# Performance work log

Hardware: AMD Instinct MI355X
Metric: run time of the kernel (lower is better)

Reference implementation:

```python
import jax, jax.numpy as jnp
import numpy as np

S, B, D, H = 256, 32, 512, 512

def setup_inputs() -> dict:
    key = jax.random.key(0)
    ks = jax.random.split(key, 14)
    return {
        "x": jax.random.normal(ks[0], (S, B, D), jnp.float32),
        "hidden_prev": jax.random.normal(ks[1], (1, B, H), jnp.float32) * 0.1,
        "Z_state": jax.random.normal(ks[2], (1, B, H, D), jnp.float32) * 0.01,
        "F_state": jax.random.normal(ks[3], (1, B, H, D), jnp.float32) * 0.01,
        "wz_state": jax.random.normal(ks[4], (1, B, H), jnp.float32) * 0.01,
        "wf_state": jax.random.normal(ks[5], (1, B, H), jnp.float32) * 0.01,
        "bz_state": jax.random.normal(ks[6], (1, B, H), jnp.float32) * 0.01,
        "bf_state": jax.random.normal(ks[7], (1, B, H), jnp.float32) * 0.01,
        "wm_z": jax.random.normal(ks[8], (H, D), jnp.float32) * 0.1,
        "wm_f": jax.random.normal(ks[9], (H, D), jnp.float32) * 0.1,
        "wv_z": jax.random.normal(ks[10], (1, H), jnp.float32) * 0.1,
        "wv_f": jax.random.normal(ks[11], (1, H), jnp.float32) * 0.1,
        "bias_z": jax.random.normal(ks[12], (1, H), jnp.float32) * 0.1,
        "bias_f": jax.random.normal(ks[13], (1, H), jnp.float32) * 0.1,
    }

def reference(x, hidden_prev, Z_state, F_state, wz_state, wf_state, bz_state, bf_state,
              wm_z, wm_f, wv_z, wv_f, bias_z, bias_f):
    # Input projections for both gates, done once: [S,B,H]
    pre_z = jnp.einsum('sbd,hd->sbh', x, wm_z)
    pre_f = jnp.einsum('sbd,hd->sbh', x, wm_f)

    def step(carry, inp):
        cell, Z, Fm, wz, wf, bz, bf = carry
        x_t, pz, pf = inp  # [B,D], [B,H], [B,H]
        z = jnp.tanh(pz + wv_z * cell + bias_z)          # [B,H]
        f = jax.nn.sigmoid(pf + wv_f * cell + bias_f)    # [B,H]
        zf = (1.0 - f) * (1.0 - z * z)
        fz = (cell - z) * (1.0 - f) * f
        common = f + zf * wv_z + fz * wv_f
        # RTRL sensitivity updates (outer products over [B,H,D])
        Zn = common[..., None] * Z + zf[..., None] * x_t[:, None, :]
        Fn = common[..., None] * Fm + fz[..., None] * x_t[:, None, :]
        wzn = cell * zf + common * wz
        wfn = cell * fz + common * wf
        bzn = zf + common * bz
        bfn = fz + common * bf
        new_cell = cell * f + (1.0 - f) * z
        return (new_cell, Zn, Fn, wzn, wfn, bzn, bfn), new_cell

    carry0 = (hidden_prev[0], Z_state[0], F_state[0],
              wz_state[0], wf_state[0], bz_state[0], bf_state[0])
    carry, cells = jax.lax.scan(step, carry0, (x, pre_z, pre_f))
    new_cell, Zn, Fn, wzn, wfn, bzn, bfn = carry
    return (cells, new_cell[None], Zn[None], Fn[None],
            wzn[None], wfn[None], bzn[None], bfn[None])
```

## Files before the change

### kernel.cpp

```cpp
#include <hip/hip_runtime.h>
#include <hip/hip_bf16.h>
#include <math.h>

namespace {

typedef short short8 __attribute__((ext_vector_type(8)));
typedef float floatx4 __attribute__((ext_vector_type(4)));
typedef unsigned int uint32;
typedef unsigned short u16;
typedef unsigned long long u64;

constexpr int S = 256, B = 32, D = 512, H = 512;
constexpr int BH = B * H;
constexpr int M1 = S * B;
constexpr int SBH = S * BH;

__device__ __forceinline__ int swz(int row, int col8) {
  return row * 64 + (col8 ^ ((row & 7) << 3));
}

__device__ __forceinline__ uint32 pkbf(float lo, float hi) {
  __hip_bfloat162 h = __float22bfloat162_rn(make_float2(lo, hi));
  uint32 r;
  __builtin_memcpy(&r, &h, 4);
  return r;
}

__device__ __forceinline__ float fast_sigmoid(float x) {
  float e = __expf(-x);
  return __builtin_amdgcn_rcpf(1.0f + e);
}
__device__ __forceinline__ float fast_tanh(float x) {
  float e = __expf(-2.0f * x);
  return fmaf(2.0f, __builtin_amdgcn_rcpf(1.0f + e), -1.0f);
}

__global__ __launch_bounds__(256) void proj_gemm(
    const float* __restrict__ x, const float* __restrict__ wmz,
    const float* __restrict__ wmf, float2* __restrict__ pzf) {
  __shared__ u16 As[128 * 64];
  __shared__ u16 Bzs[64 * 64];
  __shared__ u16 Bfs[64 * 64];
  const int tid = threadIdx.x;
  const int m0 = blockIdx.x * 128;
  const int n0 = blockIdx.y * 64;
  const int w = tid >> 6, l = tid & 63;
  const int lr = l & 15, lg = l >> 4;
  floatx4 accz[2][4], accf[2][4];
#pragma unroll
  for (int m = 0; m < 2; ++m)
#pragma unroll
    for (int n = 0; n < 4; ++n) {
      accz[m][n] = 0;
      accf[m][n] = 0;
    }
  const int sr = tid >> 3;
  const int sc = (tid & 7) * 8;
  for (int k0 = 0; k0 < D; k0 += 64) {
    __syncthreads();
#pragma unroll
    for (int p = 0; p < 4; ++p) {
      const int r = sr + 32 * p;
      const float* xp = &x[(size_t)(m0 + r) * D + k0 + sc];
      float4 a = *(const float4*)xp;
      float4 b = *(const float4*)(xp + 4);
      uint4 o;
      o.x = pkbf(a.x, a.y);
      o.y = pkbf(a.z, a.w);
      o.z = pkbf(b.x, b.y);
      o.w = pkbf(b.z, b.w);
      *(uint4*)&As[swz(r, sc)] = o;
    }
#pragma unroll
    for (int p = 0; p < 2; ++p) {
      const int r = sr + 32 * p;
      const float* zp = &wmz[(size_t)(n0 + r) * D + k0 + sc];
      float4 a = *(const float4*)zp;
      float4 b = *(const float4*)(zp + 4);
      uint4 o;
      o.x = pkbf(a.x, a.y);
      o.y = pkbf(a.z, a.w);
      o.z = pkbf(b.x, b.y);
      o.w = pkbf(b.z, b.w);
      *(uint4*)&Bzs[swz(r, sc)] = o;
      const float* fp = &wmf[(size_t)(n0 + r) * D + k0 + sc];
      float4 c = *(const float4*)fp;
      float4 d = *(const float4*)(fp + 4);
      uint4 q;
      q.x = pkbf(c.x, c.y);
      q.y = pkbf(c.z, c.w);
      q.z = pkbf(d.x, d.y);
      q.w = pkbf(d.z, d.w);
      *(uint4*)&Bfs[swz(r, sc)] = q;
    }
    __syncthreads();
    __builtin_amdgcn_s_setprio(1);
#pragma unroll
    for (int kk = 0; kk < 2; ++kk) {
      const int kb = kk * 32 + lg * 8;
      short8 a0 = *(const short8*)&As[swz(32 * w + lr, kb)];
      short8 a1 = *(const short8*)&As[swz(32 * w + 16 + lr, kb)];
#pragma unroll
      for (int n = 0; n < 4; ++n) {
        short8 bz = *(const short8*)&Bzs[swz(16 * n + lr, kb)];
        short8 bf = *(const short8*)&Bfs[swz(16 * n + lr, kb)];
        accz[0][n] = __builtin_amdgcn_mfma_f32_16x16x32_bf16(a0, bz, accz[0][n], 0, 0, 0);
        accz[1][n] = __builtin_amdgcn_mfma_f32_16x16x32_bf16(a1, bz, accz[1][n], 0, 0, 0);
        accf[0][n] = __builtin_amdgcn_mfma_f32_16x16x32_bf16(a0, bf, accf[0][n], 0, 0, 0);
        accf[1][n] = __builtin_amdgcn_mfma_f32_16x16x32_bf16(a1, bf, accf[1][n], 0, 0, 0);
      }
    }
    __builtin_amdgcn_s_setprio(0);
  }
#pragma unroll
  for (int m = 0; m < 2; ++m)
#pragma unroll
    for (int n = 0; n < 4; ++n)
#pragma unroll
      for (int j = 0; j < 4; ++j) {
        int row = m0 + 32 * w + 16 * m + lg * 4 + j;
        int col = n0 + 16 * n + lr;
        pzf[(size_t)row * H + col] = make_float2(accz[m][n][j], accf[m][n][j]);
      }
}

#define STEP_BODY(J)                                                       \
    const float z = fast_tanh(fmaf(wvz, cell, pzv));                       \
    const float f = fast_sigmoid(fmaf(wvf, cell, pfv));                    \
    const float zf = (1.0f - f) * (1.0f - z * z);                          \
    const float fz = (cell - z) * (1.0f - f) * f;                          \
    const float common = f + zf * wvz + fz * wvf;                          \
    wz = fmaf(common, wz, cell * zf);                                      \
    wf = fmaf(common, wf, cell * fz);                                      \
    bz = fmaf(common, bz, zf);                                             \
    bf = fmaf(common, bf, fz);                                             \
    cell = fmaf(f, cell - z, z);                                           \
    const size_t ti = (size_t)(t0 + (J)) * BH;                             \
    __builtin_nontemporal_store(cell, cp + ti);                            \
    pz[ti] = make_float2(__uint_as_float(pkbf(zf, fz)), common);

#define STEP_L(J, Q)                                                       \
  {                                                                        \
    const float pzv = Q.x + bsz, pfv = Q.y + bsf;                          \
    Q = pz[(size_t)(t0 + 16 + (J)) * BH];                                  \
    STEP_BODY(J)                                                           \
  }

#define STEP_N(J, Q)                                                       \
  {                                                                        \
    const float pzv = Q.x + bsz, pfv = Q.y + bsf;                          \
    STEP_BODY(J)                                                           \
  }

__global__ __launch_bounds__(64, 1) void scan_fwd(
    const float* __restrict__ hidden_prev, const float* __restrict__ wz0,
    const float* __restrict__ wf0, const float* __restrict__ bz0,
    const float* __restrict__ bf0, const float* __restrict__ wvz_,
    const float* __restrict__ wvf_, const float* __restrict__ bsz_,
    const float* __restrict__ bsf_, float2* pzf_,
    float* __restrict__ out_cells, float* __restrict__ out_newcell,
    float* __restrict__ out_wzn, float* __restrict__ out_wfn,
    float* __restrict__ out_bzn, float* __restrict__ out_bfn) {
  const int bh = blockIdx.x * 64 + threadIdx.x;
  const int h = bh & (H - 1);
  float cell = hidden_prev[bh];
  float wz = wz0[bh], wf = wf0[bh], bz = bz0[bh], bf = bf0[bh];
  const float wvz = wvz_[h], wvf = wvf_[h], bsz = bsz_[h], bsf = bsf_[h];
  float2* pz = pzf_ + bh;
  float* cp = out_cells + bh;

  float2 q0 = pz[(size_t)0 * BH], q1 = pz[(size_t)1 * BH];
  float2 q2 = pz[(size_t)2 * BH], q3 = pz[(size_t)3 * BH];
  float2 q4 = pz[(size_t)4 * BH], q5 = pz[(size_t)5 * BH];
  float2 q6 = pz[(size_t)6 * BH], q7 = pz[(size_t)7 * BH];
  float2 q8 = pz[(size_t)8 * BH], q9 = pz[(size_t)9 * BH];
  float2 q10 = pz[(size_t)10 * BH], q11 = pz[(size_t)11 * BH];
  float2 q12 = pz[(size_t)12 * BH], q13 = pz[(size_t)13 * BH];
  float2 q14 = pz[(size_t)14 * BH], q15 = pz[(size_t)15 * BH];

  for (int t0 = 0; t0 < S - 16; t0 += 16) {
    STEP_L(0, q0)  STEP_L(1, q1)  STEP_L(2, q2)  STEP_L(3, q3)
    STEP_L(4, q4)  STEP_L(5, q5)  STEP_L(6, q6)  STEP_L(7, q7)
    STEP_L(8, q8)  STEP_L(9, q9)  STEP_L(10, q10) STEP_L(11, q11)
    STEP_L(12, q12) STEP_L(13, q13) STEP_L(14, q14) STEP_L(15, q15)
  }
  {
    const int t0 = S - 16;
    STEP_N(0, q0)  STEP_N(1, q1)  STEP_N(2, q2)  STEP_N(3, q3)
    STEP_N(4, q4)  STEP_N(5, q5)  STEP_N(6, q6)  STEP_N(7, q7)
    STEP_N(8, q8)  STEP_N(9, q9)  STEP_N(10, q10) STEP_N(11, q11)
    STEP_N(12, q12) STEP_N(13, q13) STEP_N(14, q14) STEP_N(15, q15)
  }
  out_newcell[bh] = cell;
  out_wzn[bh] = wz;
  out_wfn[bh] = wf;
  out_bzn[bh] = bz;
  out_bfn[bh] = bf;
}

__global__ __launch_bounds__(1024) void suffix_kernel(
    const float2* __restrict__ pzfc, const float* __restrict__ x,
    u16* __restrict__ XT, u16* __restrict__ AzT, u16* __restrict__ AfT,
    float* __restrict__ P0_out) {
  __shared__ union {
    struct {
      float prods[16][65];
      uint32 tl[S * 65];
    } s;
    float xp[4][64][65];
  } u;
  const int tid = threadIdx.x;
  const int bh_l = tid & 63;
  const int c = tid >> 6;

  {
    const int team = tid >> 8;
    const int tt = tid & 255;
    const int tile = blockIdx.x * 4 + team;
    const int b = tile >> 5;
    const int rem = tile & 31;
    const int d0 = (rem >> 2) * 64;
    const int s0 = (rem & 3) * 64;
    const int r = tt >> 4;
    const int c4 = (tt & 15) * 4;
#pragma unroll
    for (int p = 0; p < 4; ++p) {
      const int rr = r + p * 16;
      float4 v = *(const float4*)&x[(size_t)(s0 + rr) * (B * D) +
                                    (size_t)b * D + d0 + c4];
      u.xp[team][c4 + 0][rr] = v.x;
      u.xp[team][c4 + 1][rr] = v.y;
      u.xp[team][c4 + 2][rr] = v.z;
      u.xp[team][c4 + 3][rr] = v.w;
    }
    __syncthreads();
#pragma unroll
    for (int p = 0; p < 4; ++p) {
      const int dr = r + p * 16;
      u64 o = (u64)pkbf(u.xp[team][dr][c4 + 0], u.xp[team][dr][c4 + 1]) |
              ((u64)pkbf(u.xp[team][dr][c4 + 2], u.xp[team][dr][c4 + 3]) << 32);
      *(u64*)&XT[((size_t)b * D + d0 + dr) * S + s0 + c4] = o;
    }
  }
  __syncthreads();

  const int bh = blockIdx.x * 64 + bh_l;
  const float2* p = pzfc + bh;
  float2 v[16];
#pragma unroll
  for (int i = 0; i < 16; ++i) v[i] = p[(size_t)(c * 16 + i) * BH];
  float L = 1.0f;
#pragma unroll
  for (int i = 0; i < 16; ++i) L *= v[i].y;
  u.s.prods[c][bh_l] = L;
  __syncthreads();
  float run = 1.0f;
#pragma unroll
  for (int cc = 1; cc < 16; ++cc)
    if (cc > c) run *= u.s.prods[cc][bh_l];
#pragma unroll
  for (int i = 15; i >= 0; --i) {
    const int t = c * 16 + i;
    const uint32 w32 = __float_as_uint(v[i].x);
    const float zf = __uint_as_float((w32 & 0xffffu) << 16);
    const float fz = __uint_as_float(w32 & 0xffff0000u);
    u.s.tl[t * 65 + bh_l] = pkbf(zf * run, fz * run);
    run *= v[i].y;
  }
  if (c == 0) P0_out[bh] = run;
  __syncthreads();

  const size_t base = (size_t)blockIdx.x * 64 * S;
  const int rot = (bh_l >> 3) & 3;
#pragma unroll
  for (int it = 0; it < 4; ++it) {
    const int qi = it * 1024 + tid;
    const int r = qi >> 6;
    const int qt = (qi & 63) * 4;
    uint32 a[4];
#pragma unroll
    for (int m = 0; m < 4; ++m) {
      const int k = (m + rot) & 3;
      a[k] = u.s.tl[(qt + k) * 65 + r];
    }
    u64 lo = (u64)(a[0] & 0xffffu) | ((u64)(a[1] & 0xffffu) << 16) |
             ((u64)(a[2] & 0xffffu) << 32) | ((u64)(a[3] & 0xffffu) << 48);
    u64 hi = (u64)(a[0] >> 16) | ((u64)(a[1] >> 16) << 16) |
             ((u64)(a[2] >> 16) << 32) | ((u64)(a[3] >> 16) << 48);
    *(u64*)&AzT[base + (size_t)r * S + qt] = lo;
    *(u64*)&AfT[base + (size_t)r * S + qt] = hi;
  }
}

__global__ __launch_bounds__(256, 3) void out_gemm(
    const u16* __restrict__ AzT, const u16* __restrict__ AfT,
    const u16* __restrict__ XT, const float* __restrict__ P0,
    const float* __restrict__ Z0, const float* __restrict__ F0,
    float* __restrict__ Zn, float* __restrict__ Fn) {
  __shared__ u16 smem[(128 + 64) * 64];
  const int tid = threadIdx.x;
  const int fid = blockIdx.x;
  const int L = (fid & 7) * 256 + (fid >> 3);
  const int d0 = (L & 7) * 64;
  const int h0 = ((L >> 3) & 3) * 128;
  const int bz = L >> 5;
  const int b = bz >> 1;
  const u16* A = ((bz & 1) ? AfT : AzT) + (size_t)b * H * S;
  const float* C0 = (bz & 1) ? F0 : Z0;
  float* Cn = (bz & 1) ? Fn : Zn;
  const u16* Xb = XT + (size_t)b * D * S;
  const int w = tid >> 6, l = tid & 63;
  const int lr = l & 15, lg = l >> 4;
  floatx4 acc[2][4];
#pragma unroll
  for (int m = 0; m < 2; ++m)
#pragma unroll
    for (int n = 0; n < 4; ++n) acc[m][n] = 0;
  const int sr = tid >> 3;
  const int sc = (tid & 7) * 8;

  short8 rA[4], rX[2];

#define OG_LOAD(T0)                                                        \
  {                                                                        \
    _Pragma("unroll") for (int p = 0; p < 4; ++p) {                        \
      const int r = sr + 32 * p;                                           \
      rA[p] = *(const short8*)&A[(size_t)(h0 + r) * S + (T0) + sc];        \
    }                                                                      \
    _Pragma("unroll") for (int p = 0; p < 2; ++p) {                        \
      const int r = sr + 32 * p;                                           \
      rX[p] = *(const short8*)&Xb[(size_t)(d0 + r) * S + (T0) + sc];       \
    }                                                                      \
  }

#define OG_WRITE()                                                         \
  {                                                                        \
    u16* As_ = smem;                                                       \
    u16* Xs_ = smem + 128 * 64;                                            \
    _Pragma("unroll") for (int p = 0; p < 4; ++p) {                        \
      const int r = sr + 32 * p;                                           \
      *(short8*)&As_[swz(r, sc)] = rA[p];                                  \
    }                                                                      \
    _Pragma("unroll") for (int p = 0; p < 2; ++p) {                        \
      const int r = sr + 32 * p;                                           \
      *(short8*)&Xs_[swz(r, sc)] = rX[p];                                  \
    }                                                                      \
  }

#define OG_COMPUTE()                                                       \
  {                                                                        \
    const u16* As_ = smem;                                                 \
    const u16* Xs_ = smem + 128 * 64;                                      \
    __builtin_amdgcn_s_setprio(1);                                         \
    _Pragma("unroll") for (int kk = 0; kk < 2; ++kk) {                     \
      const int kb = kk * 32 + lg * 8;                                     \
      short8 a0 = *(const short8*)&As_[swz(32 * w + lr, kb)];              \
      short8 a1 = *(const short8*)&As_[swz(32 * w + 16 + lr, kb)];         \
      _Pragma("unroll") for (int n = 0; n < 4; ++n) {                      \
        short8 xf = *(const short8*)&Xs_[swz(16 * n + lr, kb)];            \
        acc[0][n] = __builtin_amdgcn_mfma_f32_16x16x32_bf16(a0, xf, acc[0][n], 0, 0, 0); \
        acc[1][n] = __builtin_amdgcn_mfma_f32_16x16x32_bf16(a1, xf, acc[1][n], 0, 0, 0); \
      }                                                                    \
    }                                                                      \
    __builtin_amdgcn_s_setprio(0);                                         \
  }

  OG_LOAD(0)
  OG_WRITE()
  __syncthreads();
  OG_LOAD(64)
  OG_COMPUTE()
  __syncthreads();
  OG_WRITE()
  __syncthreads();
  OG_LOAD(128)
  OG_COMPUTE()
  __syncthreads();
  OG_WRITE()
  __syncthreads();
  OG_LOAD(192)
  OG_COMPUTE()
  __syncthreads();
  OG_WRITE()
  __syncthreads();

  floatx4 c0v[8];
  float p0v[8];
#pragma unroll
  for (int half = 0; half < 2; ++half)
#pragma unroll
    for (int i = 0; i < 4; ++i) {
      const int id = i * 256 + tid;
      const int row = half * 64 + (id >> 4);
      const int c4 = (id & 15) * 4;
      const int h = h0 + row;
      p0v[half * 4 + i] = P0[b * H + h];
      c0v[half * 4 + i] = __builtin_nontemporal_load(
          (const floatx4*)&C0[((size_t)b * H + h) * D + d0 + c4]);
    }

  OG_COMPUTE()

  float* eps = (float*)smem;
#pragma unroll
  for (int half = 0; half < 2; ++half) {
    __syncthreads();
    if ((w >> 1) == half) {
      const int lw = w & 1;
#pragma unroll
      for (int m = 0; m < 2; ++m)
#pragma unroll
        for (int n = 0; n < 4; ++n)
#pragma unroll
          for (int j = 0; j < 4; ++j) {
            const int row = 32 * lw + 16 * m + lg * 4 + j;
            eps[row * 68 + 16 * n + lr] = acc[m][n][j];
          }
    }
    __syncthreads();
#pragma unroll
    for (int i = 0; i < 4; ++i) {
      const int id = i * 256 + tid;
      const int row = id >> 4;
      const int c4 = (id & 15) * 4;
      const int h = h0 + half * 64 + row;
      const size_t gi = ((size_t)b * H + h) * D + d0 + c4;
      const floatx4 a = *(const floatx4*)&eps[row * 68 + c4];
      const int pi = half * 4 + i;
      floatx4 o;
      o[0] = fmaf(p0v[pi], c0v[pi][0], a[0]);
      o[1] = fmaf(p0v[pi], c0v[pi][1], a[1]);
      o[2] = fmaf(p0v[pi], c0v[pi][2], a[2]);
      o[3] = fmaf(p0v[pi], c0v[pi][3], a[3]);
      __builtin_nontemporal_store(o, (floatx4*)&Cn[gi]);
    }
  }
#undef OG_LOAD
#undef OG_WRITE
#undef OG_COMPUTE
}

}

extern "C" void kernel_launch(void* const* d_in, const int* in_sizes, int n_in,
                              void* d_out, int out_size, void* d_ws,
                              size_t ws_size, hipStream_t stream) {
  const float* x = (const float*)d_in[0];
  const float* hidden_prev = (const float*)d_in[1];
  const float* Z_state = (const float*)d_in[2];
  const float* F_state = (const float*)d_in[3];
  const float* wz_state = (const float*)d_in[4];
  const float* wf_state = (const float*)d_in[5];
  const float* bz_state = (const float*)d_in[6];
  const float* bf_state = (const float*)d_in[7];
  const float* wm_z = (const float*)d_in[8];
  const float* wm_f = (const float*)d_in[9];
  const float* wv_z = (const float*)d_in[10];
  const float* wv_f = (const float*)d_in[11];
  const float* bias_z = (const float*)d_in[12];
  const float* bias_f = (const float*)d_in[13];

  float2* pzf = (float2*)d_ws;
  u16* AzT = (u16*)(pzf + SBH);
  u16* AfT = AzT + SBH;
  u16* XT = AfT + SBH;
  float* P0 = (float*)(XT + SBH);

  float* out = (float*)d_out;
  float* out_cells = out;
  float* out_newcell = out + SBH;
  float* out_Zn = out_newcell + BH;
  float* out_Fn = out_Zn + (size_t)BH * D;
  float* out_wzn = out_Fn + (size_t)BH * D;
  float* out_wfn = out_wzn + BH;
  float* out_bzn = out_wfn + BH;
  float* out_bfn = out_bzn + BH;

  proj_gemm<<<dim3(M1 / 128, H / 64), 256, 0, stream>>>(x, wm_z, wm_f, pzf);
  scan_fwd<<<BH / 64, 64, 0, stream>>>(
      hidden_prev, wz_state, wf_state, bz_state, bf_state, wv_z, wv_f, bias_z,
      bias_f, pzf, out_cells, out_newcell, out_wzn, out_wfn, out_bzn,
      out_bfn);
  suffix_kernel<<<BH / 64, 1024, 0, stream>>>(pzf, x, XT, AzT, AfT, P0);
  out_gemm<<<2048, 256, 0, stream>>>(
      AzT, AfT, XT, P0, Z_state, F_state, out_Zn, out_Fn);
}
```

Measured before the change: 102.8 us.

## Overlap x transpose with scan and widen out_gemm tile to 128x128

The x-to-bf16 transpose (XT) moves out of suffix_kernel into extra wavefronts of scan_fwd. Those wavefronts do the transpose while the latency-bound single-wave scan runs, taking the transpose off the serial path. out_gemm tiles grow from 128x64 to 128x128, with half the blocks and occupancy lowered to 2, and C0/P0 are now loaded in the epilogue instead of prefetched before the last compute. In exchange the scan blocks compete for LDS and CUs, and the larger GEMM tile uses more registers and fewer blocks.

```diff
diff --git a/kernel.cpp b/kernel.cpp
--- a/kernel.cpp
+++ b/kernel.cpp
@@ -152,16 +152,50 @@
     STEP_BODY(J)                                                           \
   }
 
-__global__ __launch_bounds__(64, 1) void scan_fwd(
+__global__ __launch_bounds__(320, 1) void scan_fwd(
     const float* __restrict__ hidden_prev, const float* __restrict__ wz0,
     const float* __restrict__ wf0, const float* __restrict__ bz0,
     const float* __restrict__ bf0, const float* __restrict__ wvz_,
     const float* __restrict__ wvf_, const float* __restrict__ bsz_,
     const float* __restrict__ bsf_, float2* pzf_,
+    const float* __restrict__ x, u16* __restrict__ XT,
     float* __restrict__ out_cells, float* __restrict__ out_newcell,
     float* __restrict__ out_wzn, float* __restrict__ out_wfn,
     float* __restrict__ out_bzn, float* __restrict__ out_bfn) {
-  const int bh = blockIdx.x * 64 + threadIdx.x;
+  __shared__ float xp[4][64][65];
+  const int tid = threadIdx.x;
+  if (tid >= 64) {
+    const int wv = (tid >> 6) - 1;
+    const int l = tid & 63;
+    const int tile = blockIdx.x * 4 + wv;
+    const int b = tile >> 5;
+    const int rem = tile & 31;
+    const int d0 = (rem >> 2) * 64;
+    const int s0 = (rem & 3) * 64;
+    float* lt = &xp[wv][0][0];
+    const int rr = l >> 4;
+    const int cc = (l & 15) * 4;
+#pragma unroll
+    for (int p = 0; p < 16; ++p) {
+      const int row = rr + p * 4;
+      float4 v = *(const float4*)&x[(size_t)(s0 + row) * (B * D) +
+                                    (size_t)b * D + d0 + cc];
+      lt[(cc + 0) * 65 + row] = v.x;
+      lt[(cc + 1) * 65 + row] = v.y;
+      lt[(cc + 2) * 65 + row] = v.z;
+      lt[(cc + 3) * 65 + row] = v.w;
+    }
+    asm volatile("s_waitcnt lgkmcnt(0)" ::: "memory");
+#pragma unroll
+    for (int p = 0; p < 16; ++p) {
+      const int dr = rr + p * 4;
+      u64 o = (u64)pkbf(lt[dr * 65 + cc + 0], lt[dr * 65 + cc + 1]) |
+              ((u64)pkbf(lt[dr * 65 + cc + 2], lt[dr * 65 + cc + 3]) << 32);
+      *(u64*)&XT[((size_t)b * D + d0 + dr) * S + s0 + cc] = o;
+    }
+    return;
+  }
+  const int bh = blockIdx.x * 64 + tid;
   const int h = bh & (H - 1);
   float cell = hidden_prev[bh];
   float wz = wz0[bh], wf = wf0[bh], bz = bz0[bh], bf = bf0[bh];
@@ -199,51 +233,13 @@
 }
 
 __global__ __launch_bounds__(1024) void suffix_kernel(
-    const float2* __restrict__ pzfc, const float* __restrict__ x,
-    u16* __restrict__ XT, u16* __restrict__ AzT, u16* __restrict__ AfT,
-    float* __restrict__ P0_out) {
-  __shared__ union {
-    struct {
-      float prods[16][65];
-      uint32 tl[S * 65];
-    } s;
-    float xp[4][64][65];
-  } u;
+    const float2* __restrict__ pzfc, u16* __restrict__ AzT,
+    u16* __restrict__ AfT, float* __restrict__ P0_out) {
+  __shared__ float prods[16][65];
+  __shared__ uint32 tl[S * 65];
   const int tid = threadIdx.x;
   const int bh_l = tid & 63;
   const int c = tid >> 6;
-
-  {
-    const int team = tid >> 8;
-    const int tt = tid & 255;
-    const int tile = blockIdx.x * 4 + team;
-    const int b = tile >> 5;
-    const int rem = tile & 31;
-    const int d0 = (rem >> 2) * 64;
-    const int s0 = (rem & 3) * 64;
-    const int r = tt >> 4;
-    const int c4 = (tt & 15) * 4;
-#pragma unroll
-    for (int p = 0; p < 4; ++p) {
-      const int rr = r + p * 16;
-      float4 v = *(const float4*)&x[(size_t)(s0 + rr) * (B * D) +
-                                    (size_t)b * D + d0 + c4];
-      u.xp[team][c4 + 0][rr] = v.x;
-      u.xp[team][c4 + 1][rr] = v.y;
-      u.xp[team][c4 + 2][rr] = v.z;
-      u.xp[team][c4 + 3][rr] = v.w;
-    }
-    __syncthreads();
-#pragma unroll
-    for (int p = 0; p < 4; ++p) {
-      const int dr = r + p * 16;
-      u64 o = (u64)pkbf(u.xp[team][dr][c4 + 0], u.xp[team][dr][c4 + 1]) |
-              ((u64)pkbf(u.xp[team][dr][c4 + 2], u.xp[team][dr][c4 + 3]) << 32);
-      *(u64*)&XT[((size_t)b * D + d0 + dr) * S + s0 + c4] = o;
-    }
-  }
-  __syncthreads();
-
   const int bh = blockIdx.x * 64 + bh_l;
   const float2* p = pzfc + bh;
   float2 v[16];
@@ -252,24 +248,23 @@
   float L = 1.0f;
 #pragma unroll
   for (int i = 0; i < 16; ++i) L *= v[i].y;
-  u.s.prods[c][bh_l] = L;
+  prods[c][bh_l] = L;
   __syncthreads();
   float run = 1.0f;
 #pragma unroll
   for (int cc = 1; cc < 16; ++cc)
-    if (cc > c) run *= u.s.prods[cc][bh_l];
+    if (cc > c) run *= prods[cc][bh_l];
 #pragma unroll
   for (int i = 15; i >= 0; --i) {
     const int t = c * 16 + i;
     const uint32 w32 = __float_as_uint(v[i].x);
     const float zf = __uint_as_float((w32 & 0xffffu) << 16);
     const float fz = __uint_as_float(w32 & 0xffff0000u);
-    u.s.tl[t * 65 + bh_l] = pkbf(zf * run, fz * run);
+    tl[t * 65 + bh_l] = pkbf(zf * run, fz * run);
     run *= v[i].y;
   }
   if (c == 0) P0_out[bh] = run;
   __syncthreads();
-
   const size_t base = (size_t)blockIdx.x * 64 * S;
   const int rot = (bh_l >> 3) & 3;
 #pragma unroll
@@ -281,7 +276,7 @@
 #pragma unroll
     for (int m = 0; m < 4; ++m) {
       const int k = (m + rot) & 3;
-      a[k] = u.s.tl[(qt + k) * 65 + r];
+      a[k] = tl[(qt + k) * 65 + r];
     }
     u64 lo = (u64)(a[0] & 0xffffu) | ((u64)(a[1] & 0xffffu) << 16) |
              ((u64)(a[2] & 0xffffu) << 32) | ((u64)(a[3] & 0xffffu) << 48);
@@ -292,18 +287,18 @@
   }
 }
 
-__global__ __launch_bounds__(256, 3) void out_gemm(
+__global__ __launch_bounds__(256, 2) void out_gemm(
     const u16* __restrict__ AzT, const u16* __restrict__ AfT,
     const u16* __restrict__ XT, const float* __restrict__ P0,
     const float* __restrict__ Z0, const float* __restrict__ F0,
     float* __restrict__ Zn, float* __restrict__ Fn) {
-  __shared__ u16 smem[(128 + 64) * 64];
+  __shared__ u16 smem[(128 + 128) * 64];
   const int tid = threadIdx.x;
   const int fid = blockIdx.x;
-  const int L = (fid & 7) * 256 + (fid >> 3);
-  const int d0 = (L & 7) * 64;
-  const int h0 = ((L >> 3) & 3) * 128;
-  const int bz = L >> 5;
+  const int L = (fid & 7) * 128 + (fid >> 3);
+  const int d0 = (L & 3) * 128;
+  const int h0 = ((L >> 2) & 3) * 128;
+  const int bz = L >> 4;
   const int b = bz >> 1;
   const u16* A = ((bz & 1) ? AfT : AzT) + (size_t)b * H * S;
   const float* C0 = (bz & 1) ? F0 : Z0;
@@ -311,24 +306,21 @@
   const u16* Xb = XT + (size_t)b * D * S;
   const int w = tid >> 6, l = tid & 63;
   const int lr = l & 15, lg = l >> 4;
-  floatx4 acc[2][4];
+  floatx4 acc[2][8];
 #pragma unroll
   for (int m = 0; m < 2; ++m)
 #pragma unroll
-    for (int n = 0; n < 4; ++n) acc[m][n] = 0;
+    for (int n = 0; n < 8; ++n) acc[m][n] = 0;
   const int sr = tid >> 3;
   const int sc = (tid & 7) * 8;
 
-  short8 rA[4], rX[2];
+  short8 rA[4], rX[4];
 
 #define OG_LOAD(T0)                                                        \
   {                                                                        \
     _Pragma("unroll") for (int p = 0; p < 4; ++p) {                        \
       const int r = sr + 32 * p;                                           \
       rA[p] = *(const short8*)&A[(size_t)(h0 + r) * S + (T0) + sc];        \
-    }                                                                      \
-    _Pragma("unroll") for (int p = 0; p < 2; ++p) {                        \
-      const int r = sr + 32 * p;                                           \
       rX[p] = *(const short8*)&Xb[(size_t)(d0 + r) * S + (T0) + sc];       \
     }                                                                      \
   }
@@ -340,9 +332,6 @@
     _Pragma("unroll") for (int p = 0; p < 4; ++p) {                        \
       const int r = sr + 32 * p;                                           \
       *(short8*)&As_[swz(r, sc)] = rA[p];                                  \
-    }                                                                      \
-    _Pragma("unroll") for (int p = 0; p < 2; ++p) {                        \
-      const int r = sr + 32 * p;                                           \
       *(short8*)&Xs_[swz(r, sc)] = rX[p];                                  \
     }                                                                      \
   }
@@ -356,7 +345,7 @@
       const int kb = kk * 32 + lg * 8;                                     \
       short8 a0 = *(const short8*)&As_[swz(32 * w + lr, kb)];              \
       short8 a1 = *(const short8*)&As_[swz(32 * w + 16 + lr, kb)];         \
-      _Pragma("unroll") for (int n = 0; n < 4; ++n) {                      \
+      _Pragma("unroll") for (int n = 0; n < 8; ++n) {                      \
         short8 xf = *(const short8*)&Xs_[swz(16 * n + lr, kb)];            \
         acc[0][n] = __builtin_amdgcn_mfma_f32_16x16x32_bf16(a0, xf, acc[0][n], 0, 0, 0); \
         acc[1][n] = __builtin_amdgcn_mfma_f32_16x16x32_bf16(a1, xf, acc[1][n], 0, 0, 0); \
@@ -383,55 +372,39 @@
   __syncthreads();
   OG_WRITE()
   __syncthreads();
-
-  floatx4 c0v[8];
-  float p0v[8];
-#pragma unroll
-  for (int half = 0; half < 2; ++half)
-#pragma unroll
-    for (int i = 0; i < 4; ++i) {
-      const int id = i * 256 + tid;
-      const int row = half * 64 + (id >> 4);
-      const int c4 = (id & 15) * 4;
-      const int h = h0 + row;
-      p0v[half * 4 + i] = P0[b * H + h];
-      c0v[half * 4 + i] = __builtin_nontemporal_load(
-          (const floatx4*)&C0[((size_t)b * H + h) * D + d0 + c4]);
-    }
-
   OG_COMPUTE()
 
   float* eps = (float*)smem;
 #pragma unroll
-  for (int half = 0; half < 2; ++half) {
+  for (int q = 0; q < 4; ++q) {
     __syncthreads();
-    if ((w >> 1) == half) {
-      const int lw = w & 1;
+    if (w == q) {
 #pragma unroll
       for (int m = 0; m < 2; ++m)
 #pragma unroll
-        for (int n = 0; n < 4; ++n)
+        for (int n = 0; n < 8; ++n)
 #pragma unroll
           for (int j = 0; j < 4; ++j) {
-            const int row = 32 * lw + 16 * m + lg * 4 + j;
-            eps[row * 68 + 16 * n + lr] = acc[m][n][j];
+            const int row = 16 * m + lg * 4 + j;
+            eps[row * 132 + 16 * n + lr] = acc[m][n][j];
           }
     }
     __syncthreads();
 #pragma unroll
-    for (int i = 0; i < 4; ++i) {
-      const int id = i * 256 + tid;
-      const int row = id >> 4;
-      const int c4 = (id & 15) * 4;
-      const int h = h0 + half * 64 + row;
+    for (int it = 0; it < 4; ++it) {
+      const int id = it * 256 + tid;
+      const int row = id >> 5;
+      const int c4 = (id & 31) * 4;
+      const int h = h0 + q * 32 + row;
+      const float p0 = P0[b * H + h];
       const size_t gi = ((size_t)b * H + h) * D + d0 + c4;
-      const floatx4 a = *(const floatx4*)&eps[row * 68 + c4];
-      const int pi = half * 4 + i;
+      const floatx4 a = *(const floatx4*)&eps[row * 132 + c4];
+      const floatx4 c0 = __builtin_nontemporal_load((const floatx4*)&C0[gi]);
       floatx4 o;
-      o[0] = fmaf(p0v[pi], c0v[pi][0], a[0]);
-      o[1] = fmaf(p0v[pi], c0v[pi][1], a[1]);
-      o[2] = fmaf(p0v[pi], c0v[pi][2], a[2]);
-      o[3] = fmaf(p0v[pi], c0v[pi][3], a[3]);
+      o[0] = fmaf(p0, c0[0], a[0]);
+      o[1] = fmaf(p0, c0[1], a[1]);
+      o[2] = fmaf(p0, c0[2], a[2]);
+      o[3] = fmaf(p0, c0[3], a[3]);
       __builtin_nontemporal_store(o, (floatx4*)&Cn[gi]);
     }
   }
@@ -477,11 +450,11 @@
   float* out_bfn = out_bzn + BH;
 
   proj_gemm<<<dim3(M1 / 128, H / 64), 256, 0, stream>>>(x, wm_z, wm_f, pzf);
-  scan_fwd<<<BH / 64, 64, 0, stream>>>(
+  scan_fwd<<<BH / 64, 320, 0, stream>>>(
       hidden_prev, wz_state, wf_state, bz_state, bf_state, wv_z, wv_f, bias_z,
-      bias_f, pzf, out_cells, out_newcell, out_wzn, out_wfn, out_bzn,
+      bias_f, pzf, x, XT, out_cells, out_newcell, out_wzn, out_wfn, out_bzn,
       out_bfn);
-  suffix_kernel<<<BH / 64, 1024, 0, stream>>>(pzf, x, XT, AzT, AfT, P0);
-  out_gemm<<<2048, 256, 0, stream>>>(
+  suffix_kernel<<<BH / 64, 1024, 0, stream>>>(pzf, AzT, AfT, P0);
+  out_gemm<<<1024, 256, 0, stream>>>(
       AzT, AfT, XT, P0, Z_state, F_state, out_Zn, out_Fn);
 }
```

New measurement: 97.35 us (median of 2 runs). -5.3%, faster.
